# Kernel optimization log

Measured on AMD Instinct MI355X. Metric: run time of the kernel, lower is better.

The kernel has to match this reference:

```python
import jax, jax.numpy as jnp
import numpy as np

N_NODES = 100000


def _add_self_loops(edge_index, n):
    loop = jnp.arange(n, dtype=edge_index.dtype)
    src = jnp.concatenate([edge_index[0], loop])
    dst = jnp.concatenate([edge_index[1], loop])
    return src, dst


def _gcn_conv(x, src, dst, dinv_src, dinv_dst, W, b, n):
    # linear transform first (PyG GCNConv), then normalized scatter-add
    h = x @ W                                   # [N, out]
    msg = h[src] * (dinv_src * dinv_dst)[:, None]  # [E+N, out] gather
    out = jax.ops.segment_sum(msg, dst, num_segments=n)
    return out + b


def reference(x, edge_index, W0, b0, W1, b1, Wf, bf):
    n = N_NODES
    src, dst = _add_self_loops(edge_index, n)
    ones = jnp.ones(src.shape[0], dtype=x.dtype)
    deg = jax.ops.segment_sum(ones, dst, num_segments=n)
    dinv = jnp.where(deg > 0, jax.lax.rsqrt(jnp.maximum(deg, 1.0)), 0.0)
    dinv_src = dinv[src]
    dinv_dst = dinv[dst]

    h = jax.nn.relu(_gcn_conv(x, src, dst, dinv_src, dinv_dst, W0, b0, n))
    h = jax.nn.relu(_gcn_conv(h, src, dst, dinv_src, dinv_dst, W1, b1, n))
    return h @ Wf + bf


def setup_inputs() -> dict:
    key = jax.random.key(0)
    ks = jax.random.split(key, 8)
    n, e, f, h = N_NODES, 1600000, 32, 32
    return {
        "x": jax.random.normal(ks[0], (n, f), dtype=jnp.float32),
        "edge_index": jax.random.randint(ks[1], (2, e), 0, n, dtype=jnp.int64),
        "W0": jax.random.normal(ks[2], (f, h), dtype=jnp.float32) / np.sqrt(f),
        "b0": jnp.zeros((h,), dtype=jnp.float32),
        "W1": jax.random.normal(ks[3], (h, h), dtype=jnp.float32) / np.sqrt(h),
        "b1": jnp.zeros((h,), dtype=jnp.float32),
        "Wf": jax.random.normal(ks[4], (h, h), dtype=jnp.float32) / np.sqrt(h),
        "bf": jnp.zeros((h,), dtype=jnp.float32),
    }
```

## Files before the change

kernel.cpp:

```cpp
#include <hip/hip_runtime.h>
#include <hip/hip_fp16.h>


#define GNN_F 32
#define NBKT 391
#define BCAP 5120
#define CHUNK 8192

__global__ __launch_bounds__(256) void k_fused1(
    const float* __restrict__ x, const float* __restrict__ W0,
    __half* __restrict__ t,
    const int* __restrict__ src, const int* __restrict__ dst,
    int* bcnt, int* __restrict__ queue,
    int n, int e, int gemmBlocks) {
    __shared__ float Wl[32 * 32];
    __shared__ int hist4[4 * NBKT], curs[NBKT], base[NBKT];
    int tid = threadIdx.x;

    if (blockIdx.x < gemmBlocks) {
        ((float4*)Wl)[tid] = ((const float4*)W0)[tid];
        __syncthreads();
        int r = blockIdx.x * 256 + tid;
        if (r >= n) return;
        float xr[32];
        const float4* in4 = (const float4*)(x + (size_t)r * 32);
#pragma unroll
        for (int j = 0; j < 8; ++j) {
            float4 v = in4[j];
            xr[4 * j + 0] = v.x; xr[4 * j + 1] = v.y;
            xr[4 * j + 2] = v.z; xr[4 * j + 3] = v.w;
        }
        float acc[32];
#pragma unroll
        for (int c = 0; c < 32; ++c) acc[c] = 0.0f;
#pragma unroll
        for (int k = 0; k < 32; ++k) {
            float xv = xr[k];
#pragma unroll
            for (int c = 0; c < 32; ++c) acc[c] = fmaf(xv, Wl[k * 32 + c], acc[c]);
        }
        uint4* tp = (uint4*)(t + (size_t)r * 32);
#pragma unroll
        for (int j = 0; j < 4; ++j) {
            __half2 h0 = __floats2half2_rn(acc[8 * j + 0], acc[8 * j + 1]);
            __half2 h1 = __floats2half2_rn(acc[8 * j + 2], acc[8 * j + 3]);
            __half2 h2 = __floats2half2_rn(acc[8 * j + 4], acc[8 * j + 5]);
            __half2 h3 = __floats2half2_rn(acc[8 * j + 6], acc[8 * j + 7]);
            uint4 o;
            o.x = *(unsigned*)&h0; o.y = *(unsigned*)&h1;
            o.z = *(unsigned*)&h2; o.w = *(unsigned*)&h3;
            tp[j] = o;
        }
    } else {
        int c0 = (blockIdx.x - gemmBlocks) * CHUNK;
        int g0 = c0 >> 2;
        int n4 = e >> 2;
        int cpy = (tid & 3) * NBKT;
        for (int i = tid; i < 4 * NBKT; i += 256) hist4[i] = 0;
        __syncthreads();
#pragma unroll
        for (int p = 0; p < CHUNK / 1024; ++p) {
            int g = g0 + p * 256 + tid;
            if (g < n4) {
                int4 d = ((const int4*)dst)[g];
                atomicAdd(&hist4[cpy + (((unsigned)d.x) >> 8)], 1);
                atomicAdd(&hist4[cpy + (((unsigned)d.y) >> 8)], 1);
                atomicAdd(&hist4[cpy + (((unsigned)d.z) >> 8)], 1);
                atomicAdd(&hist4[cpy + (((unsigned)d.w) >> 8)], 1);
            }
        }
        int tail0 = e & ~3;
        if (tail0 >= c0 && tail0 < c0 + CHUNK && tid < (e & 3))
            atomicAdd(&hist4[cpy + (((unsigned)dst[tail0 + tid]) >> 8)], 1);
        __syncthreads();
        for (int b = tid; b < NBKT; b += 256) {
            int h = hist4[b] + hist4[NBKT + b] + hist4[2 * NBKT + b] + hist4[3 * NBKT + b];
            base[b] = h ? atomicAdd(&bcnt[b], h) : 0;
            curs[b] = 0;
        }
        __syncthreads();
#pragma unroll
        for (int p = 0; p < CHUNK / 1024; ++p) {
            int g = g0 + p * 256 + tid;
            if (g < n4) {
                int4 d = ((const int4*)dst)[g];
                int4 sv = ((const int4*)src)[g];
                int b, l, slot;
                b = ((unsigned)d.x) >> 8; l = atomicAdd(&curs[b], 1); slot = base[b] + l;
                if (slot < BCAP) queue[(size_t)b * BCAP + slot] = (sv.x << 8) | (d.x & 255);
                b = ((unsigned)d.y) >> 8; l = atomicAdd(&curs[b], 1); slot = base[b] + l;
                if (slot < BCAP) queue[(size_t)b * BCAP + slot] = (sv.y << 8) | (d.y & 255);
                b = ((unsigned)d.z) >> 8; l = atomicAdd(&curs[b], 1); slot = base[b] + l;
                if (slot < BCAP) queue[(size_t)b * BCAP + slot] = (sv.z << 8) | (d.z & 255);
                b = ((unsigned)d.w) >> 8; l = atomicAdd(&curs[b], 1); slot = base[b] + l;
                if (slot < BCAP) queue[(size_t)b * BCAP + slot] = (sv.w << 8) | (d.w & 255);
            }
        }
        if (tail0 >= c0 && tail0 < c0 + CHUNK && tid < (e & 3)) {
            int j = tail0 + tid;
            int d = dst[j];
            int b = ((unsigned)d) >> 8;
            int l = atomicAdd(&curs[b], 1);
            int slot = base[b] + l;
            if (slot < BCAP) queue[(size_t)b * BCAP + slot] = (src[j] << 8) | (d & 255);
        }
    }
}

__global__ __launch_bounds__(256) void k_build(
    const int* __restrict__ bcnt, const int* __restrict__ queue,
    int* __restrict__ csr, int* __restrict__ rs, float* __restrict__ dinv,
    __half* __restrict__ t, int n) {
    __shared__ int red[256];
    __shared__ int hist2[2 * 256], sh[256], cur[256];
    __shared__ float dsh[256];
    int b = blockIdx.x;
    int tid = threadIdx.x;

    int part = 0;
    for (int i = tid; i < b; i += 256) {
        int v = bcnt[i];
        part += (v > BCAP ? BCAP : v);
    }
    red[tid] = part;
    hist2[tid] = 0;
    hist2[256 + tid] = 0;
    __syncthreads();
#pragma unroll
    for (int off = 128; off > 0; off >>= 1) {
        if (tid < off) red[tid] += red[tid + off];
        __syncthreads();
    }
    int bbase = red[0];

    int len = bcnt[b];
    if (len > BCAP) len = BCAP;
    const int* q = queue + (size_t)b * BCAP;

    int cpy = (tid & 1) << 8;
    for (int i = tid; i < len; i += 256) atomicAdd(&hist2[cpy + (q[i] & 255)], 1);
    __syncthreads();
    int c = hist2[tid] + hist2[256 + tid];
    sh[tid] = c;
    __syncthreads();
    for (int off = 1; off < 256; off <<= 1) {
        int xv = (tid >= off) ? sh[tid - off] : 0;
        __syncthreads();
        sh[tid] += xv;
        __syncthreads();
    }
    int myStart = bbase + sh[tid] - c;
    int node = (b << 8) + tid;
    float dv = rsqrtf((float)(c + 1));
    if (node < n) {
        rs[node] = myStart;
        dinv[node] = dv;
    }
    if (b == (int)gridDim.x - 1 && tid == 255) rs[n] = myStart + c;
    dsh[tid] = dv;
    cur[tid] = myStart;
    __syncthreads();
    for (int i = tid; i < len; i += 256) {
        int qq = q[i];
        int p = atomicAdd(&cur[qq & 255], 1);
        csr[p] = ((unsigned)qq) >> 8;
    }
    int rows = n - (b << 8);
    if (rows > 256) rows = 256;
    if (rows < 0) rows = 0;
    uint4* t4 = (uint4*)(t + ((size_t)b << 8) * 32);
    for (int i = tid; i < rows * 4; i += 256) {
        float d = dsh[i >> 2];
        uint4 v = t4[i];
        __half2 h0 = *(__half2*)&v.x, h1 = *(__half2*)&v.y;
        __half2 h2 = *(__half2*)&v.z, h3 = *(__half2*)&v.w;
        float2 f0 = __half22float2(h0), f1 = __half22float2(h1);
        float2 f2 = __half22float2(h2), f3 = __half22float2(h3);
        h0 = __floats2half2_rn(f0.x * d, f0.y * d);
        h1 = __floats2half2_rn(f1.x * d, f1.y * d);
        h2 = __floats2half2_rn(f2.x * d, f2.y * d);
        h3 = __floats2half2_rn(f3.x * d, f3.y * d);
        v.x = *(unsigned*)&h0; v.y = *(unsigned*)&h1;
        v.z = *(unsigned*)&h2; v.w = *(unsigned*)&h3;
        t4[i] = v;
    }
}

#define LOAD4(u, A, B)                                         \
    {                                                          \
        uint2 raw = ((const uint2*)(t + (size_t)(u) * 32))[j]; \
        __half2 p0 = *(__half2*)&raw.x;                        \
        __half2 p1 = *(__half2*)&raw.y;                        \
        A = __half22float2(p0);                                \
        B = __half22float2(p1);                                \
    }

#define GATHER_BODY()                                                          \
    int idx = blockIdx.x * 256 + threadIdx.x;                                  \
    int tid = threadIdx.x;                                                     \
    int row = idx >> 3;                                                        \
    bool live = row < n;                                                       \
    if (!live) row = n - 1;                                                    \
    int j = tid & 7;                                                           \
    ((float4*)Wl)[tid] = ((const float4*)W)[tid];                              \
    __syncthreads();                                                           \
    int e0 = rs[row];                                                          \
    int e1 = rs[row + 1];                                                      \
    float ax = 0.f, ay = 0.f, az = 0.f, aw = 0.f;                              \
    int e = e0;                                                                \
    int rem = e1 - e0;                                                         \
    int u0, u1, u2, u3, u4, u5, u6, u7;                                        \
    if (rem >= 8) {                                                            \
        u0 = csr[e];     u1 = csr[e + 1]; u2 = csr[e + 2]; u3 = csr[e + 3];    \
        u4 = csr[e + 4]; u5 = csr[e + 5]; u6 = csr[e + 6]; u7 = csr[e + 7];    \
    }                                                                          \
    while (rem >= 8) {                                                         \
        float2 a0, b0v, a1, b1v, a2, b2v, a3, b3v;                             \
        float2 a4, b4v, a5, b5v, a6, b6v, a7, b7v;                             \
        LOAD4(u0, a0, b0v); LOAD4(u1, a1, b1v);                                \
        LOAD4(u2, a2, b2v); LOAD4(u3, a3, b3v);                                \
        LOAD4(u4, a4, b4v); LOAD4(u5, a5, b5v);                                \
        LOAD4(u6, a6, b6v); LOAD4(u7, a7, b7v);                                \
        e += 8; rem -= 8;                                                      \
        if (rem >= 8) {                                                        \
            u0 = csr[e];     u1 = csr[e + 1]; u2 = csr[e + 2]; u3 = csr[e + 3];\
            u4 = csr[e + 4]; u5 = csr[e + 5]; u6 = csr[e + 6]; u7 = csr[e + 7];\
        }                                                                      \
        ax += ((a0.x + a1.x) + (a2.x + a3.x)) + ((a4.x + a5.x) + (a6.x + a7.x));\
        ay += ((a0.y + a1.y) + (a2.y + a3.y)) + ((a4.y + a5.y) + (a6.y + a7.y));\
        az += ((b0v.x + b1v.x) + (b2v.x + b3v.x)) + ((b4v.x + b5v.x) + (b6v.x + b7v.x));\
        aw += ((b0v.y + b1v.y) + (b2v.y + b3v.y)) + ((b4v.y + b5v.y) + (b6v.y + b7v.y));\
    }                                                                          \
    for (; e < e1; ++e) {                                                      \
        int u = csr[e];                                                        \
        float2 a, bb;                                                          \
        LOAD4(u, a, bb);                                                       \
        ax += a.x; ay += a.y; az += bb.x; aw += bb.y;                          \
    }                                                                          \
    float2 sa, sb;                                                             \
    LOAD4(row, sa, sb);                                                        \
    float d = dinv[row];                                                       \
    float4 pb4 = ((const float4*)preb)[j];                                     \
    float4 u4v;                                                                \
    u4v.x = fmaxf(d * (ax + sa.x) + pb4.x, 0.0f);                              \
    u4v.y = fmaxf(d * (ay + sa.y) + pb4.y, 0.0f);                              \
    u4v.z = fmaxf(d * (az + sb.x) + pb4.z, 0.0f);                              \
    u4v.w = fmaxf(d * (aw + sb.y) + pb4.w, 0.0f);                              \
    int wv = tid >> 6;                                                         \
    int g = (tid >> 3) & 7;                                                    \
    float* urow = ur + wv * 320 + g * 40;                                      \
    *(float4*)(urow + 4 * j) = u4v;                                            \
    __syncthreads();

__global__ __launch_bounds__(256) void k_gather_gemm(
    const int* __restrict__ rs, const int* __restrict__ csr,
    const float* __restrict__ dinv, const __half* __restrict__ t,
    const float* __restrict__ W, const float* __restrict__ preb,
    __half* __restrict__ t_out, int n) {
    __shared__ float Wl[32 * 32];
    __shared__ float ur[4 * 320];
    GATHER_BODY()
    float4 o = make_float4(0.f, 0.f, 0.f, 0.f);
#pragma unroll
    for (int k = 0; k < 32; ++k) {
        float uk = urow[k];
        float4 wv4 = ((const float4*)(Wl + k * 32))[j];
        o.x = fmaf(uk, wv4.x, o.x);
        o.y = fmaf(uk, wv4.y, o.y);
        o.z = fmaf(uk, wv4.z, o.z);
        o.w = fmaf(uk, wv4.w, o.w);
    }
    o.x *= d; o.y *= d; o.z *= d; o.w *= d;
    if (live) {
        __half2 h0 = __floats2half2_rn(o.x, o.y);
        __half2 h1 = __floats2half2_rn(o.z, o.w);
        uint2 pk;
        pk.x = *(unsigned*)&h0; pk.y = *(unsigned*)&h1;
        ((uint2*)(t_out + (size_t)row * 32))[j] = pk;
    }
}

__global__ __launch_bounds__(256) void k_gather_out(
    const int* __restrict__ rs, const int* __restrict__ csr,
    const float* __restrict__ dinv, const __half* __restrict__ t,
    const float* __restrict__ W, const float* __restrict__ preb,
    const float* __restrict__ postb, float* __restrict__ out, int n) {
    __shared__ float Wl[32 * 32];
    __shared__ float ur[4 * 320];
    GATHER_BODY()
    float4 o = ((const float4*)postb)[j];
#pragma unroll
    for (int k = 0; k < 32; ++k) {
        float uk = urow[k];
        float4 wv4 = ((const float4*)(Wl + k * 32))[j];
        o.x = fmaf(uk, wv4.x, o.x);
        o.y = fmaf(uk, wv4.y, o.y);
        o.z = fmaf(uk, wv4.z, o.z);
        o.w = fmaf(uk, wv4.w, o.w);
    }
    if (live) ((float4*)(out + (size_t)row * 32))[j] = o;
}

extern "C" void kernel_launch(void* const* d_in, const int* in_sizes, int n_in,
                              void* d_out, int out_size, void* d_ws, size_t ws_size,
                              hipStream_t stream) {
    const float* x  = (const float*)d_in[0];
    const int*   ei = (const int*)d_in[1];
    const float* W0 = (const float*)d_in[2];
    const float* b0 = (const float*)d_in[3];
    const float* W1 = (const float*)d_in[4];
    const float* b1 = (const float*)d_in[5];
    const float* Wf = (const float*)d_in[6];
    const float* bf = (const float*)d_in[7];
    float* out = (float*)d_out;

    const int N = in_sizes[0] / GNN_F;
    const int E = in_sizes[1] / 2;
    const int* srcI = ei;
    const int* dstI = ei + E;

    const int gN = (N + 255) / 256;
    const int gG = (N * 8 + 255) / 256;
    const int nChunk = (E + CHUNK - 1) / CHUNK;

    char* ws = (char*)d_ws;
    size_t off = 0;
    auto alloc = [&](size_t bytes) {
        void* p = ws + off;
        off += (bytes + 127) & ~(size_t)127;
        return p;
    };
    int*    bcnt  = (int*)alloc((size_t)NBKT * 4);
    int*    rs    = (int*)alloc((size_t)(N + 1) * 4);
    float*  dinv  = (float*)alloc((size_t)N * 4);
    int*    queue = (int*)alloc((size_t)NBKT * BCAP * 4);
    int*    csr   = (int*)alloc((size_t)E * 4);
    __half* t_a   = (__half*)alloc((size_t)N * GNN_F * 2);
    __half* t_b   = (__half*)alloc((size_t)N * GNN_F * 2);
    (void)ws_size;

    hipMemsetAsync(bcnt, 0, (size_t)NBKT * 4, stream);

    k_fused1<<<gN + nChunk, 256, 0, stream>>>(x, W0, t_a, srcI, dstI, bcnt,
                                              queue, N, E, gN);
    k_build<<<NBKT, 256, 0, stream>>>(bcnt, queue, csr, rs, dinv, t_a, N);

    k_gather_gemm<<<gG, 256, 0, stream>>>(rs, csr, dinv, t_a, W1, b0, t_b, N);

    k_gather_out<<<gG, 256, 0, stream>>>(rs, csr, dinv, t_b, Wf, b1, bf, out, N);
}
```

Baseline: 170.6 us.

## Pad feature buffers with a zero sentinel row to remove the gather tail loop

Measured after the change: 162.6 us. -4.7%, faster.

```diff
diff --git a/kernel.cpp b/kernel.cpp
--- a/kernel.cpp
+++ b/kernel.cpp
@@ -18,6 +18,10 @@
     int tid = threadIdx.x;
 
     if (blockIdx.x < gemmBlocks) {
+        if (blockIdx.x == 0 && tid < 4) {
+            uint4 z = make_uint4(0u, 0u, 0u, 0u);
+            ((uint4*)(t + (size_t)n * 32))[tid] = z;
+        }
         ((float4*)Wl)[tid] = ((const float4*)W0)[tid];
         __syncthreads();
         int r = blockIdx.x * 256 + tid;
@@ -195,6 +199,14 @@
         B = __half22float2(p1);                                \
     }
 
+#define GIDX(k_, uvar)                       \
+    {                                        \
+        int ik = e + (k_);                   \
+        bool ok = ik < e1;                   \
+        uvar = csr[ok ? ik : last];          \
+        uvar = ok ? uvar : n;                \
+    }
+
 #define GATHER_BODY()                                                          \
     int idx = blockIdx.x * 256 + threadIdx.x;                                  \
     int tid = threadIdx.x;                                                     \
@@ -202,19 +214,24 @@
     bool live = row < n;                                                       \
     if (!live) row = n - 1;                                                    \
     int j = tid & 7;                                                           \
+    int e0 = rs[row];                                                          \
+    int e1 = rs[row + 1];                                                      \
     ((float4*)Wl)[tid] = ((const float4*)W)[tid];                              \
     __syncthreads();                                                           \
-    int e0 = rs[row];                                                          \
-    int e1 = rs[row + 1];                                                      \
+    int last = e1 - 1;                                                         \
+    float2 sa, sb;                                                             \
+    LOAD4(row, sa, sb);                                                        \
+    float d = dinv[row];                                                       \
     float ax = 0.f, ay = 0.f, az = 0.f, aw = 0.f;                              \
     int e = e0;                                                                \
     int rem = e1 - e0;                                                         \
     int u0, u1, u2, u3, u4, u5, u6, u7;                                        \
-    if (rem >= 8) {                                                            \
-        u0 = csr[e];     u1 = csr[e + 1]; u2 = csr[e + 2]; u3 = csr[e + 3];    \
-        u4 = csr[e + 4]; u5 = csr[e + 5]; u6 = csr[e + 6]; u7 = csr[e + 7];    \
+    if (rem > 0) {                                                             \
+        u0 = csr[e];                                                           \
+        GIDX(1, u1) GIDX(2, u2) GIDX(3, u3)                                    \
+        GIDX(4, u4) GIDX(5, u5) GIDX(6, u6) GIDX(7, u7)                        \
     }                                                                          \
-    while (rem >= 8) {                                                         \
+    while (rem > 0) {                                                          \
         float2 a0, b0v, a1, b1v, a2, b2v, a3, b3v;                             \
         float2 a4, b4v, a5, b5v, a6, b6v, a7, b7v;                             \
         LOAD4(u0, a0, b0v); LOAD4(u1, a1, b1v);                                \
@@ -222,24 +239,16 @@
         LOAD4(u4, a4, b4v); LOAD4(u5, a5, b5v);                                \
         LOAD4(u6, a6, b6v); LOAD4(u7, a7, b7v);                                \
         e += 8; rem -= 8;                                                      \
-        if (rem >= 8) {                                                        \
-            u0 = csr[e];     u1 = csr[e + 1]; u2 = csr[e + 2]; u3 = csr[e + 3];\
-            u4 = csr[e + 4]; u5 = csr[e + 5]; u6 = csr[e + 6]; u7 = csr[e + 7];\
+        if (rem > 0) {                                                         \
+            u0 = csr[e];                                                       \
+            GIDX(1, u1) GIDX(2, u2) GIDX(3, u3)                                \
+            GIDX(4, u4) GIDX(5, u5) GIDX(6, u6) GIDX(7, u7)                    \
         }                                                                      \
         ax += ((a0.x + a1.x) + (a2.x + a3.x)) + ((a4.x + a5.x) + (a6.x + a7.x));\
         ay += ((a0.y + a1.y) + (a2.y + a3.y)) + ((a4.y + a5.y) + (a6.y + a7.y));\
         az += ((b0v.x + b1v.x) + (b2v.x + b3v.x)) + ((b4v.x + b5v.x) + (b6v.x + b7v.x));\
         aw += ((b0v.y + b1v.y) + (b2v.y + b3v.y)) + ((b4v.y + b5v.y) + (b6v.y + b7v.y));\
     }                                                                          \
-    for (; e < e1; ++e) {                                                      \
-        int u = csr[e];                                                        \
-        float2 a, bb;                                                          \
-        LOAD4(u, a, bb);                                                       \
-        ax += a.x; ay += a.y; az += bb.x; aw += bb.y;                          \
-    }                                                                          \
-    float2 sa, sb;                                                             \
-    LOAD4(row, sa, sb);                                                        \
-    float d = dinv[row];                                                       \
     float4 pb4 = ((const float4*)preb)[j];                                     \
     float4 u4v;                                                                \
     u4v.x = fmaxf(d * (ax + sa.x) + pb4.x, 0.0f);                              \
@@ -250,7 +259,9 @@
     int g = (tid >> 3) & 7;                                                    \
     float* urow = ur + wv * 320 + g * 40;                                      \
     *(float4*)(urow + 4 * j) = u4v;                                            \
-    __syncthreads();
+       \
+                \
+    asm volatile("s_waitcnt lgkmcnt(0)" ::: "memory");
 
 __global__ __launch_bounds__(256) void k_gather_gemm(
     const int* __restrict__ rs, const int* __restrict__ csr,
@@ -259,6 +270,10 @@
     __half* __restrict__ t_out, int n) {
     __shared__ float Wl[32 * 32];
     __shared__ float ur[4 * 320];
+    if (blockIdx.x == 0 && threadIdx.x < 4) {
+        uint4 z = make_uint4(0u, 0u, 0u, 0u);
+        ((uint4*)(t_out + (size_t)n * 32))[threadIdx.x] = z;
+    }
     GATHER_BODY()
     float4 o = make_float4(0.f, 0.f, 0.f, 0.f);
 #pragma unroll
@@ -335,8 +350,8 @@
     float*  dinv  = (float*)alloc((size_t)N * 4);
     int*    queue = (int*)alloc((size_t)NBKT * BCAP * 4);
     int*    csr   = (int*)alloc((size_t)E * 4);
-    __half* t_a   = (__half*)alloc((size_t)N * GNN_F * 2);
-    __half* t_b   = (__half*)alloc((size_t)N * GNN_F * 2);
+    __half* t_a   = (__half*)alloc((size_t)(N + 1) * GNN_F * 2);
+    __half* t_b   = (__half*)alloc((size_t)(N + 1) * GNN_F * 2);
     (void)ws_size;
 
     hipMemsetAsync(bcnt, 0, (size_t)NBKT * 4, stream);
```
